# Kernel tuning notes

Hardware: AMD Instinct MI355X
Metric: run time of the kernel (lower is better)

## Reference

```python
import jax, jax.numpy as jnp
import numpy as np

N_HEADS = 16


def setup_inputs() -> dict:
    key = jax.random.key(0)
    ks = jax.random.split(key, 5)
    B, S, D = 4, 1024, 1024
    H = N_HEADS
    hs = D // H
    sc = 0.02
    return {
        "x": jax.random.normal(ks[0], (B, S, D), jnp.float32),
        "Wqkv": jax.random.normal(ks[1], (3 * D, D), jnp.float32) * sc,
        "Wout": jax.random.normal(ks[2], (D, D), jnp.float32) * sc,
        "Wpos": jax.random.normal(ks[3], (D, D), jnp.float32) * sc,
        "posn_vect_u": jnp.zeros((1, H, 1, hs), jnp.float32),
        "posn_vect_v": jnp.zeros((1, H, 1, hs), jnp.float32),
        "rel_embed": jax.random.normal(ks[4], (S, D), jnp.float32) * sc,
    }


def reference(x, Wqkv, Wout, Wpos, posn_vect_u, posn_vect_v, rel_embed):
    B, S, D = x.shape
    H = N_HEADS
    hs = D // H

    # qkv projection (torch Linear: y = x @ W.T), split into q,k,v
    qkv = x @ Wqkv.T  # [B,S,3D]
    q, k, v = jnp.split(qkv, 3, axis=-1)
    # [B,S,D] -> [B,H,S,hs]
    q = q.reshape(B, S, H, hs).transpose(0, 2, 1, 3)
    k = k.reshape(B, S, H, hs).transpose(0, 2, 1, 3)
    v = v.reshape(B, S, H, hs).transpose(0, 2, 1, 3)

    # content term: (q + u) @ k^T -> [B,H,S,S]
    attn_dots = jnp.einsum("bhqd,bhkd->bhqk", q + posn_vect_u, k)

    # relative position term (Transformer-XL style)
    rel = rel_embed[-S:] @ Wpos.T          # [S,D]
    rel = rel.T.reshape(H, hs, S)          # [H,hs,S]
    query_posn = jnp.einsum("bhqd,hdk->bhqk", q + posn_vect_v, rel)  # [B,H,S,S]

    # rel-shift gather: shifted[i,j] = query_posn[i, j - i + S - 1]
    i = jnp.arange(S)[:, None]
    j = jnp.arange(S)[None, :]
    idx = jnp.clip(j - i + S - 1, 0, S - 1)  # [S,S]; entries with j>i masked later
    shifted = jnp.take_along_axis(query_posn, idx[None, None], axis=-1)
    attn_dots = attn_dots + shifted

    # causal mask then scaled softmax (matches masked_fill then softmax(x/sqrt(hs)))
    causal = j > i  # [S,S] True above diagonal
    attn_dots = jnp.where(causal[None, None], -jnp.inf, attn_dots)
    scores = jax.nn.softmax(attn_dots / np.sqrt(hs).astype(np.float32), axis=-1)

    attn = jnp.einsum("bhqk,bhkd->bhqd", scores, v)  # [B,H,S,hs]
    out = attn.transpose(0, 2, 1, 3).reshape(B, S, D) @ Wout.T
    return out
```

## Files before the change

kernel.cpp:

```cpp
#include <hip/hip_runtime.h>

#define S_LEN 1024

typedef unsigned short u16;
using bf16x8 = __attribute__((ext_vector_type(8))) short;
using f32x4  = __attribute__((ext_vector_type(4))) float;
using u16x8  = __attribute__((ext_vector_type(8))) unsigned short;
using u16x4  = __attribute__((ext_vector_type(4))) unsigned short;
using u32x4  = __attribute__((ext_vector_type(4))) unsigned int;

__device__ __forceinline__ float bf2f(u16 b) {
  unsigned int u = ((unsigned int)b) << 16;
  return __builtin_bit_cast(float, u);
}
__device__ __forceinline__ u16 f2bf(float f) {
  unsigned int u = __builtin_bit_cast(unsigned int, f);
  unsigned int r = u + 0x7fffu + ((u >> 16) & 1u);
  return (u16)(r >> 16);
}
__device__ __forceinline__ unsigned int cvtpk(float lo, float hi) {
  unsigned int r;
  asm("v_cvt_pk_bf16_f32 %0, %1, %2" : "=v"(r) : "v"(lo), "v"(hi));
  return r;
}
__device__ __forceinline__ float fmax3(float a, float b, float c) {
  return fmaxf(fmaxf(a, b), c);
}

using gas_p = const __attribute__((address_space(1))) void*;
using las_p = __attribute__((address_space(3))) void*;
__device__ __forceinline__ void gload16(const void* g, void* l) {
  __builtin_amdgcn_global_load_lds((gas_p)g, (las_p)l, 16, 0, 0);
}

__global__ __launch_bounds__(256) void cvt_all(const float* __restrict__ x,
    const float* __restrict__ wqkv, const float* __restrict__ wout,
    const float* __restrict__ wpos, const float* __restrict__ rel,
    u16* __restrict__ xb, u16* __restrict__ wqkvb, u16* __restrict__ woutb,
    u16* __restrict__ wposb, u16* __restrict__ relb) {
  int blk = blockIdx.x;
  const float* src; u16* dst; int base;
  if (blk < 4096)      { src = x;    dst = xb;    base = blk; }
  else if (blk < 7168) { src = wqkv; dst = wqkvb; base = blk - 4096; }
  else if (blk < 8192) { src = wout; dst = woutb; base = blk - 7168; }
  else if (blk < 9216) { src = wpos; dst = wposb; base = blk - 8192; }
  else                 { src = rel;  dst = relb;  base = blk - 9216; }
  int i = (base * 256 + threadIdx.x) * 4;
  float4 v = *(const float4*)(src + i);
  u16x4 o;
  o.x = f2bf(v.x); o.y = f2bf(v.y); o.z = f2bf(v.z); o.w = f2bf(v.w);
  *(u16x4*)(dst + i) = o;
}

__global__ __launch_bounds__(256) void gemm_qkv_rel(
    const u16* __restrict__ xb, const u16* __restrict__ wqkvb,
    u16* __restrict__ qkvb, u16* __restrict__ qc, u16* __restrict__ qp,
    const float* __restrict__ uvec, const float* __restrict__ vvec,
    const u16* __restrict__ relb, const u16* __restrict__ wposb,
    u16* __restrict__ relproj) {
  __shared__ __align__(16) u16 As[2][128 * 32];
  __shared__ __align__(16) u16 Ws[2][128 * 32];
  const int t = threadIdx.x;
  const int w = t >> 6, l = t & 63;
  const int lr = l & 15, lg = l >> 4;
  const int flat = blockIdx.x;

  if (flat < 768) {
    const int xcd = flat & 7, idx = flat >> 3;
    const int bm = (xcd & 3) * 8 + (idx & 7);
    const int bn = (xcd >> 2) * 12 + (idx >> 3);
    const int wr = (w >> 1) * 64, wc = (w & 1) * 64;
    f32x4 acc[4][4];
#pragma unroll
    for (int mi = 0; mi < 4; ++mi)
#pragma unroll
      for (int ni = 0; ni < 4; ++ni) acc[mi][ni] = (f32x4){0.f, 0.f, 0.f, 0.f};
    const u16* Ab = xb + (size_t)bm * 128 * 1024;
    const u16* Wb = wqkvb + (size_t)bn * 128 * 1024;
    auto stage = [&](int k0, int buf) {
#pragma unroll
      for (int i = 0; i < 2; ++i) {
        int c = i * 256 + t;
        gload16(Ab + (size_t)(c >> 2) * 1024 + k0 + (c & 3) * 8, &As[buf][c * 8]);
      }
#pragma unroll
      for (int i = 0; i < 2; ++i) {
        int c = i * 256 + t;
        gload16(Wb + (size_t)(c >> 2) * 1024 + k0 + (c & 3) * 8, &Ws[buf][c * 8]);
      }
    };
    stage(0, 0);
    __syncthreads();
    for (int k0 = 0; k0 < 1024; k0 += 32) {
      const int cur = (k0 >> 5) & 1;
      if (k0 + 32 < 1024) stage(k0 + 32, cur ^ 1);
      bf16x8 af[4], wf[4];
#pragma unroll
      for (int mi = 0; mi < 4; ++mi)
        af[mi] = *(const bf16x8*)&As[cur][(wr + mi * 16 + lr) * 32 + lg * 8];
#pragma unroll
      for (int ni = 0; ni < 4; ++ni)
        wf[ni] = *(const bf16x8*)&Ws[cur][(wc + ni * 16 + lr) * 32 + lg * 8];
      __builtin_amdgcn_s_setprio(1);
#pragma unroll
      for (int mi = 0; mi < 4; ++mi)
#pragma unroll
        for (int ni = 0; ni < 4; ++ni)
          acc[mi][ni] = __builtin_amdgcn_mfma_f32_16x16x32_bf16(af[mi], wf[ni], acc[mi][ni], 0, 0, 0);
      __builtin_amdgcn_s_setprio(0);
      __syncthreads();
    }
#pragma unroll
    for (int mi = 0; mi < 4; ++mi)
#pragma unroll
      for (int ni = 0; ni < 4; ++ni) {
        int col = bn * 128 + wc + ni * 16 + lr;
        if (col < 1024) {
          float uu = uvec[col], vv = vvec[col];
#pragma unroll
          for (int g = 0; g < 4; ++g) {
            int row = bm * 128 + wr + mi * 16 + lg * 4 + g;
            qc[(size_t)row * 1024 + col] = f2bf((acc[mi][ni][g] + uu) * 0.125f);
            qp[(size_t)row * 1024 + col] = f2bf((acc[mi][ni][g] + vv) * 0.125f);
          }
        } else if (col < 2048) {
#pragma unroll
          for (int g = 0; g < 4; ++g) {
            int row = bm * 128 + wr + mi * 16 + lg * 4 + g;
            qkvb[(size_t)row * 3072 + col] = f2bf(acc[mi][ni][g]);
          }
        } else {
          int row0 = bm * 128 + wr + mi * 16 + lg * 4;
          int vrow = (row0 >> 10) * 1024 + (col - 2048);
          u16x4 tmp;
#pragma unroll
          for (int g = 0; g < 4; ++g) tmp[g] = f2bf(acc[mi][ni][g]);
          *(u16x4*)&qkvb[(size_t)vrow * 3072 + (row0 & 1023)] = tmp;
        }
      }
  } else {
    const int r = flat - 768;
    const int bm = r & 15, bn = r >> 4;
    const int wr = (w >> 1) * 32, wc = (w & 1) * 64;
    f32x4 acc[2][4];
#pragma unroll
    for (int mi = 0; mi < 2; ++mi)
#pragma unroll
      for (int ni = 0; ni < 4; ++ni) acc[mi][ni] = (f32x4){0.f, 0.f, 0.f, 0.f};
    const u16* Ab = relb + (size_t)bm * 64 * 1024;
    const u16* Wb = wposb + (size_t)bn * 128 * 1024;
    auto stage = [&](int k0, int buf) {
      {
        int c = t;
        gload16(Ab + (size_t)(c >> 2) * 1024 + k0 + (c & 3) * 8, &As[buf][c * 8]);
      }
#pragma unroll
      for (int i = 0; i < 2; ++i) {
        int c = i * 256 + t;
        gload16(Wb + (size_t)(c >> 2) * 1024 + k0 + (c & 3) * 8, &Ws[buf][c * 8]);
      }
    };
    stage(0, 0);
    __syncthreads();
    for (int k0 = 0; k0 < 1024; k0 += 32) {
      const int cur = (k0 >> 5) & 1;
      if (k0 + 32 < 1024) stage(k0 + 32, cur ^ 1);
      bf16x8 af[2], wf[4];
#pragma unroll
      for (int mi = 0; mi < 2; ++mi)
        af[mi] = *(const bf16x8*)&As[cur][(wr + mi * 16 + lr) * 32 + lg * 8];
#pragma unroll
      for (int ni = 0; ni < 4; ++ni)
        wf[ni] = *(const bf16x8*)&Ws[cur][(wc + ni * 16 + lr) * 32 + lg * 8];
      __builtin_amdgcn_s_setprio(1);
#pragma unroll
      for (int mi = 0; mi < 2; ++mi)
#pragma unroll
        for (int ni = 0; ni < 4; ++ni)
          acc[mi][ni] = __builtin_amdgcn_mfma_f32_16x16x32_bf16(af[mi], wf[ni], acc[mi][ni], 0, 0, 0);
      __builtin_amdgcn_s_setprio(0);
      __syncthreads();
    }
#pragma unroll
    for (int mi = 0; mi < 2; ++mi)
#pragma unroll
      for (int ni = 0; ni < 4; ++ni) {
        int col = bn * 128 + wc + ni * 16 + lr;
#pragma unroll
        for (int g = 0; g < 4; ++g) {
          int row = bm * 64 + wr + mi * 16 + lg * 4 + g;
          relproj[(size_t)row * 1024 + col] = f2bf(acc[mi][ni][g]);
        }
      }
  }
}

__global__ __launch_bounds__(256) void gemm_out(const u16* __restrict__ A,
    const u16* __restrict__ W, float* __restrict__ Yf) {
  __shared__ __align__(16) u16 As[2][64 * 32];
  __shared__ __align__(16) u16 Ws[2][128 * 32];
  const int t = threadIdx.x;
  const int w = t >> 6, l = t & 63;
  const int lr = l & 15, lg = l >> 4;
  const int flat = (int)blockIdx.y * 64 + (int)blockIdx.x;
  const int bn = flat & 7, bm = flat >> 3;
  const int wr = (w >> 1) * 32, wc = (w & 1) * 64;
  f32x4 acc[2][4];
#pragma unroll
  for (int mi = 0; mi < 2; ++mi)
#pragma unroll
    for (int ni = 0; ni < 4; ++ni) acc[mi][ni] = (f32x4){0.f, 0.f, 0.f, 0.f};
  const u16* Ab = A + (size_t)bm * 64 * 1024;
  const u16* Wb = W + (size_t)bn * 128 * 1024;
  auto stage = [&](int k0, int buf) {
    {
      int c = t;
      gload16(Ab + (size_t)(c >> 2) * 1024 + k0 + (c & 3) * 8, &As[buf][c * 8]);
    }
#pragma unroll
    for (int i = 0; i < 2; ++i) {
      int c = i * 256 + t;
      gload16(Wb + (size_t)(c >> 2) * 1024 + k0 + (c & 3) * 8, &Ws[buf][c * 8]);
    }
  };
  stage(0, 0);
  __syncthreads();
  for (int k0 = 0; k0 < 1024; k0 += 32) {
    const int cur = (k0 >> 5) & 1;
    if (k0 + 32 < 1024) stage(k0 + 32, cur ^ 1);
    bf16x8 af[2], wf[4];
#pragma unroll
    for (int mi = 0; mi < 2; ++mi)
      af[mi] = *(const bf16x8*)&As[cur][(wr + mi * 16 + lr) * 32 + lg * 8];
#pragma unroll
    for (int ni = 0; ni < 4; ++ni)
      wf[ni] = *(const bf16x8*)&Ws[cur][(wc + ni * 16 + lr) * 32 + lg * 8];
    __builtin_amdgcn_s_setprio(1);
#pragma unroll
    for (int mi = 0; mi < 2; ++mi)
#pragma unroll
      for (int ni = 0; ni < 4; ++ni)
        acc[mi][ni] = __builtin_amdgcn_mfma_f32_16x16x32_bf16(af[mi], wf[ni], acc[mi][ni], 0, 0, 0);
    __builtin_amdgcn_s_setprio(0);
    __syncthreads();
  }
#pragma unroll
  for (int mi = 0; mi < 2; ++mi)
#pragma unroll
    for (int ni = 0; ni < 4; ++ni) {
      int col = bn * 128 + wc + ni * 16 + lr;
#pragma unroll
      for (int g = 0; g < 4; ++g) {
        int row = bm * 64 + wr + mi * 16 + lg * 4 + g;
        Yf[(size_t)row * 1024 + col] = acc[mi][ni][g];
      }
    }
}

__global__ __launch_bounds__(256) void attn_fwd(
    const u16* __restrict__ qcb, const u16* __restrict__ qpb,
    const u16* __restrict__ qkv, const u16* __restrict__ relp,
    u16* __restrict__ out) {
  __shared__ __align__(16) u16 Ksb[2][4096];
  __shared__ __align__(16) u16 Vtb[2][4096];
  __shared__ __align__(16) u16 Rs3[3][4096];
  __shared__ __align__(16) float Psf[4][16][68];

  const int flat = (int)blockIdx.y * 8 + (int)blockIdx.x;
  const int wg = (flat & 7) * 64 + (flat >> 3);
  const int sub = wg & 7;
  const int bh = wg >> 3;
  const int b = bh >> 4, h = bh & 15;
  const int t = threadIdx.x;
  const int w = t >> 6, l = t & 63;
  const int lr = l & 15, lg = l >> 4;

  const u16* Kg = qkv + (size_t)b * S_LEN * 3072 + 1024 + h * 64;
  const u16* Vg = qkv + (size_t)bh * 64 * 3072;
  const u16* Rg = relp + h * 64;

  int gl4[4], cg[4];
#pragma unroll
  for (int g = 0; g < 4; ++g) {
    int ql = lg * 4 + g;
    gl4[g] = (l & 48) | ((lr - ql - 1) & 15);
    cg[g] = (lr > ql) ? 1 : 0;
  }

  for (int half = 0; half < 2; ++half) {
    const int qt = half ? sub : (15 - sub);
    const int i0 = qt * 64;
    const int nt = qt + 1;

    bf16x8 qcf[2], qpf[2];
    {
      size_t qoff = (size_t)(b * S_LEN + i0 + w * 16 + lr) * 1024 + h * 64;
      qcf[0] = *(const bf16x8*)(qcb + qoff + lg * 8);
      qcf[1] = *(const bf16x8*)(qcb + qoff + 32 + lg * 8);
      qpf[0] = *(const bf16x8*)(qpb + qoff + lg * 8);
      qpf[1] = *(const bf16x8*)(qpb + qoff + 32 + lg * 8);
    }

    auto stage_k = [&](int j0s, int buf) {
#pragma unroll
      for (int i = 0; i < 2; ++i) {
        int bK = i * 4 + w;
        int ttk = bK >> 1, kc = bK & 1;
        gload16(Kg + (size_t)(j0s + ttk * 16 + lr) * 3072 + kc * 32 + lg * 8,
                &Ksb[buf][bK * 512 + l * 8]);
      }
    };
    auto stage_v = [&](int j0s, int buf) {
#pragma unroll
      for (int i = 0; i < 2; ++i) {
        int bV = i * 4 + w;
        int dt = bV >> 1, kc = bV & 1;
        gload16(Vg + (size_t)(dt * 16 + lr) * 3072 + j0s + kc * 32 + lg * 8,
                &Vtb[buf][bV * 512 + l * 8]);
      }
    };
    auto stage_rchunk = [&](int Gloc, int slot) {
      int Gg = 15 - qt + Gloc;
#pragma unroll
      for (int i = 0; i < 2; ++i) {
        int bR = i * 4 + w;
        int btc = bR >> 1, kc = bR & 1;
        int r = Gg * 64 + btc * 16 + lr;
        r = r > S_LEN - 1 ? S_LEN - 1 : r;
        gload16(Rg + (size_t)r * 1024 + kc * 32 + lg * 8,
                &Rs3[slot][bR * 512 + l * 8]);
      }
    };

    float m_run = 0.f, l_run = 0.f;
    f32x4 o_acc[4];
#pragma unroll
    for (int dt = 0; dt < 4; ++dt) o_acc[dt] = (f32x4){0.f, 0.f, 0.f, 0.f};

    stage_k(0, 0);
    stage_v(0, 0);
    stage_rchunk(0, 0);
    stage_rchunk(1, 1);
    __syncthreads();

    int sA = 0, sB = 1, sC = 2;
    for (int kt = 0; kt < nt; ++kt) {
      const int cur = kt & 1, nxt = cur ^ 1;
      const int j0 = kt * 64;
      const int have_nxt = (kt + 1 < nt);
      if (have_nxt) {
        stage_k(j0 + 64, nxt);
        stage_v(j0 + 64, nxt);
        stage_rchunk(kt + 2, sC);
      }

      f32x4 sc[4];
      __builtin_amdgcn_s_setprio(1);
#pragma unroll
      for (int tt = 0; tt < 4; ++tt) {
        sc[tt] = (f32x4){0.f, 0.f, 0.f, 0.f};
#pragma unroll
        for (int kc = 0; kc < 2; ++kc) {
          bf16x8 kf = *(const bf16x8*)&Ksb[cur][(tt * 2 + kc) * 512 + l * 8];
          sc[tt] = __builtin_amdgcn_mfma_f32_16x16x32_bf16(qcf[kc], kf, sc[tt], 0, 0, 0);
        }
      }
      f32x4 sp[5];
#pragma unroll
      for (int u5 = 0; u5 < 5; ++u5) {
        int bt = 3 - w + u5;
        const u16* rb = (bt & 4) ? &Rs3[sB][0] : &Rs3[sA][0];
        int btc = bt & 3;
        sp[u5] = (f32x4){0.f, 0.f, 0.f, 0.f};
#pragma unroll
        for (int kc = 0; kc < 2; ++kc) {
          bf16x8 rf = *(const bf16x8*)&rb[(btc * 2 + kc) * 512 + l * 8];
          sp[u5] = __builtin_amdgcn_mfma_f32_16x16x32_bf16(qpf[kc], rf, sp[u5], 0, 0, 0);
        }
      }
      __builtin_amdgcn_s_setprio(0);

#pragma unroll
      for (int g = 0; g < 4; ++g) {
        float bp[5];
#pragma unroll
        for (int u5 = 0; u5 < 5; ++u5) bp[u5] = __shfl(sp[u5][g], gl4[g]);
#pragma unroll
        for (int tt = 0; tt < 4; ++tt)
          sc[tt][g] += cg[g] ? bp[tt + 1] : bp[tt];
      }
#pragma unroll
      for (int g = 0; g < 4; ++g)
#pragma unroll
        for (int tt = 0; tt < 4; ++tt)
          Psf[w][lg * 4 + g][tt * 16 + lr] = sc[tt][g];

      float zz[2][8];
#pragma unroll
      for (int kc = 0; kc < 2; ++kc)
#pragma unroll
        for (int h4 = 0; h4 < 2; ++h4) {
          float4 rv = *(const float4*)&Psf[w][lr][kc * 32 + lg * 8 + h4 * 4];
          zz[kc][h4 * 4 + 0] = rv.x; zz[kc][h4 * 4 + 1] = rv.y;
          zz[kc][h4 * 4 + 2] = rv.z; zz[kc][h4 * 4 + 3] = rv.w;
        }
      if (kt == nt - 1) {
        int iglob = i0 + w * 16 + lr;
#pragma unroll
        for (int kc = 0; kc < 2; ++kc)
#pragma unroll
          for (int j = 0; j < 8; ++j)
            if (j0 + kc * 32 + lg * 8 + j > iglob) zz[kc][j] = -1e30f;
      }

#pragma unroll
      for (int kc = 0; kc < 2; ++kc)
#pragma unroll
        for (int j = 0; j < 8; ++j) zz[kc][j] = __expf(zz[kc][j] - m_run);
      bf16x8 pf[2];
#pragma unroll
      for (int kc = 0; kc < 2; ++kc) {
        u32x4 pw;
#pragma unroll
        for (int j2 = 0; j2 < 4; ++j2)
          pw[j2] = cvtpk(zz[kc][j2 * 2], zz[kc][j2 * 2 + 1]);
        pf[kc] = __builtin_bit_cast(bf16x8, pw);
      }
      __builtin_amdgcn_s_setprio(1);
#pragma unroll
      for (int dt = 0; dt < 4; ++dt) {
#pragma unroll
        for (int kc = 0; kc < 2; ++kc) {
          bf16x8 vf = *(const bf16x8*)&Vtb[cur][(dt * 2 + kc) * 512 + l * 8];
          o_acc[dt] = __builtin_amdgcn_mfma_f32_16x16x32_bf16(pf[kc], vf, o_acc[dt], 0, 0, 0);
        }
      }
      __builtin_amdgcn_s_setprio(0);

      float s, em;
      {
        float a0 = zz[0][0] + zz[0][1], a1 = zz[0][2] + zz[0][3];
        float a2 = zz[0][4] + zz[0][5], a3 = zz[0][6] + zz[0][7];
        float a4 = zz[1][0] + zz[1][1], a5 = zz[1][2] + zz[1][3];
        float a6 = zz[1][4] + zz[1][5], a7 = zz[1][6] + zz[1][7];
        s = ((a0 + a1) + (a2 + a3)) + ((a4 + a5) + (a6 + a7));
        float m0 = fmax3(zz[0][0], zz[0][1], zz[0][2]);
        float m1 = fmax3(zz[0][3], zz[0][4], zz[0][5]);
        float m2 = fmax3(zz[0][6], zz[0][7], zz[1][0]);
        float m3 = fmax3(zz[1][1], zz[1][2], zz[1][3]);
        float m4 = fmax3(zz[1][4], zz[1][5], zz[1][6]);
        em = fmax3(m0, m1, zz[1][7]);
        em = fmax3(em, m2, m3);
        em = fmaxf(em, m4);
      }
      s += __shfl_xor(s, 16);
      s += __shfl_xor(s, 32);
      em = fmaxf(em, __shfl_xor(em, 16));
      em = fmaxf(em, __shfl_xor(em, 32));

      if (__all(em <= 2980.958f)) {
        l_run += s;
      } else {
        float lem = __logf(fmaxf(em, 1.f));
        float corr = __expf(-lem);
        m_run += lem;
        l_run = (l_run + s) * corr;
        float co[4];
#pragma unroll
        for (int g = 0; g < 4; ++g) co[g] = __shfl(corr, lg * 4 + g);
#pragma unroll
        for (int dt = 0; dt < 4; ++dt)
#pragma unroll
          for (int g = 0; g < 4; ++g) o_acc[dt][g] *= co[g];
      }

      __syncthreads();
      int stmp = sA; sA = sB; sB = sC; sC = stmp;
    }

    float ll[4];
#pragma unroll
    for (int g = 0; g < 4; ++g) ll[g] = __shfl(l_run, lg * 4 + g);
#pragma unroll
    for (int dt = 0; dt < 4; ++dt) {
      int col = h * 64 + dt * 16 + lr;
#pragma unroll
      for (int g = 0; g < 4; ++g) {
        int row = b * S_LEN + i0 + w * 16 + lg * 4 + g;
        out[(size_t)row * 1024 + col] = f2bf(o_acc[dt][g] / ll[g]);
      }
    }
  }
}

extern "C" void kernel_launch(void* const* d_in, const int* in_sizes, int n_in,
                              void* d_out, int out_size, void* d_ws, size_t ws_size,
                              hipStream_t stream) {
  const float* x    = (const float*)d_in[0];
  const float* Wqkv = (const float*)d_in[1];
  const float* Wout = (const float*)d_in[2];
  const float* Wpos = (const float*)d_in[3];
  const float* u    = (const float*)d_in[4];
  const float* v    = (const float*)d_in[5];
  const float* rel  = (const float*)d_in[6];
  float* out = (float*)d_out;

  u16* ws      = (u16*)d_ws;
  u16* xb      = ws;
  u16* wqkvb   = xb + 4194304;
  u16* woutb   = wqkvb + 3145728;
  u16* wposb   = woutb + 1048576;
  u16* relb    = wposb + 1048576;
  u16* qkvb    = relb + 1048576;
  u16* qcb     = qkvb + 12582912;
  u16* qpb     = qcb + 4194304;
  u16* relproj = qpb + 4194304;
  u16* attno   = relproj + 1048576;

  cvt_all<<<10240, 256, 0, stream>>>(x, Wqkv, Wout, Wpos, rel, xb, wqkvb, woutb, wposb, relb);

  gemm_qkv_rel<<<896, 256, 0, stream>>>(xb, wqkvb, qkvb, qcb, qpb, u, v, relb, wposb, relproj);
  attn_fwd<<<dim3(8, 64), 256, 0, stream>>>(qcb, qpb, qkvb, relproj, attno);
  gemm_out<<<dim3(64, 8), 256, 0, stream>>>(attno, woutb, out);
}
```

Baseline: 126.6 us.

## Software-pipeline score MFMAs one tile ahead of softmax and PV

```diff
diff --git a/kernel.cpp b/kernel.cpp
--- a/kernel.cpp
+++ b/kernel.cpp
@@ -332,68 +332,75 @@
       }
     };
 
+    f32x4 sc[4], sp[5];
+    auto compute_tile = [&](int ti) {
+      __builtin_amdgcn_s_setprio(1);
+#pragma unroll
+      for (int tt = 0; tt < 4; ++tt) {
+        sc[tt] = (f32x4){0.f, 0.f, 0.f, 0.f};
+#pragma unroll
+        for (int kc = 0; kc < 2; ++kc) {
+          bf16x8 kf = *(const bf16x8*)&Ksb[ti & 1][(tt * 2 + kc) * 512 + l * 8];
+          sc[tt] = __builtin_amdgcn_mfma_f32_16x16x32_bf16(qcf[kc], kf, sc[tt], 0, 0, 0);
+        }
+      }
+      const u16* rbA = &Rs3[ti % 3][0];
+      const u16* rbB = &Rs3[(ti + 1) % 3][0];
+#pragma unroll
+      for (int u5 = 0; u5 < 5; ++u5) {
+        int bt = 3 - w + u5;
+        const u16* rb = (bt & 4) ? rbB : rbA;
+        int btc = bt & 3;
+        sp[u5] = (f32x4){0.f, 0.f, 0.f, 0.f};
+#pragma unroll
+        for (int kc = 0; kc < 2; ++kc) {
+          bf16x8 rf = *(const bf16x8*)&rb[(btc * 2 + kc) * 512 + l * 8];
+          sp[u5] = __builtin_amdgcn_mfma_f32_16x16x32_bf16(qpf[kc], rf, sp[u5], 0, 0, 0);
+        }
+      }
+      __builtin_amdgcn_s_setprio(0);
+    };
+    auto gather_write = [&](int ti) {
+      const int j0t = ti * 64;
+      const int diag = (ti == nt - 1);
+#pragma unroll
+      for (int g = 0; g < 4; ++g) {
+        float bp[5];
+#pragma unroll
+        for (int u5 = 0; u5 < 5; ++u5) bp[u5] = __shfl(sp[u5][g], gl4[g]);
+        int ql = lg * 4 + g;
+#pragma unroll
+        for (int tt = 0; tt < 4; ++tt) {
+          float z = sc[tt][g] + (cg[g] ? bp[tt + 1] : bp[tt]);
+          if (diag && (j0t + tt * 16 + lr > i0 + w * 16 + ql)) z = -1e30f;
+          Psf[w][ql][tt * 16 + lr] = z;
+        }
+      }
+    };
+
     float m_run = 0.f, l_run = 0.f;
     f32x4 o_acc[4];
 #pragma unroll
     for (int dt = 0; dt < 4; ++dt) o_acc[dt] = (f32x4){0.f, 0.f, 0.f, 0.f};
 
     stage_k(0, 0);
+    stage_k(64, 1);
     stage_v(0, 0);
     stage_rchunk(0, 0);
     stage_rchunk(1, 1);
+    stage_rchunk(2, 2);
     __syncthreads();
-
-    int sA = 0, sB = 1, sC = 2;
+    compute_tile(0);
+    gather_write(0);
+    __syncthreads();
+
     for (int kt = 0; kt < nt; ++kt) {
-      const int cur = kt & 1, nxt = cur ^ 1;
       const int j0 = kt * 64;
-      const int have_nxt = (kt + 1 < nt);
-      if (have_nxt) {
-        stage_k(j0 + 64, nxt);
-        stage_v(j0 + 64, nxt);
-        stage_rchunk(kt + 2, sC);
-      }
-
-      f32x4 sc[4];
-      __builtin_amdgcn_s_setprio(1);
-#pragma unroll
-      for (int tt = 0; tt < 4; ++tt) {
-        sc[tt] = (f32x4){0.f, 0.f, 0.f, 0.f};
-#pragma unroll
-        for (int kc = 0; kc < 2; ++kc) {
-          bf16x8 kf = *(const bf16x8*)&Ksb[cur][(tt * 2 + kc) * 512 + l * 8];
-          sc[tt] = __builtin_amdgcn_mfma_f32_16x16x32_bf16(qcf[kc], kf, sc[tt], 0, 0, 0);
-        }
-      }
-      f32x4 sp[5];
-#pragma unroll
-      for (int u5 = 0; u5 < 5; ++u5) {
-        int bt = 3 - w + u5;
-        const u16* rb = (bt & 4) ? &Rs3[sB][0] : &Rs3[sA][0];
-        int btc = bt & 3;
-        sp[u5] = (f32x4){0.f, 0.f, 0.f, 0.f};
-#pragma unroll
-        for (int kc = 0; kc < 2; ++kc) {
-          bf16x8 rf = *(const bf16x8*)&rb[(btc * 2 + kc) * 512 + l * 8];
-          sp[u5] = __builtin_amdgcn_mfma_f32_16x16x32_bf16(qpf[kc], rf, sp[u5], 0, 0, 0);
-        }
-      }
-      __builtin_amdgcn_s_setprio(0);
-
-#pragma unroll
-      for (int g = 0; g < 4; ++g) {
-        float bp[5];
-#pragma unroll
-        for (int u5 = 0; u5 < 5; ++u5) bp[u5] = __shfl(sp[u5][g], gl4[g]);
-#pragma unroll
-        for (int tt = 0; tt < 4; ++tt)
-          sc[tt][g] += cg[g] ? bp[tt + 1] : bp[tt];
-      }
-#pragma unroll
-      for (int g = 0; g < 4; ++g)
-#pragma unroll
-        for (int tt = 0; tt < 4; ++tt)
-          Psf[w][lg * 4 + g][tt * 16 + lr] = sc[tt][g];
+      if (kt + 2 < nt) {
+        stage_k(j0 + 128, kt & 1);
+        stage_rchunk(kt + 3, kt % 3);
+      }
+      if (kt + 1 < nt) stage_v(j0 + 64, (kt + 1) & 1);
 
       float zz[2][8];
 #pragma unroll
@@ -404,15 +411,6 @@
           zz[kc][h4 * 4 + 0] = rv.x; zz[kc][h4 * 4 + 1] = rv.y;
           zz[kc][h4 * 4 + 2] = rv.z; zz[kc][h4 * 4 + 3] = rv.w;
         }
-      if (kt == nt - 1) {
-        int iglob = i0 + w * 16 + lr;
-#pragma unroll
-        for (int kc = 0; kc < 2; ++kc)
-#pragma unroll
-          for (int j = 0; j < 8; ++j)
-            if (j0 + kc * 32 + lg * 8 + j > iglob) zz[kc][j] = -1e30f;
-      }
-
 #pragma unroll
       for (int kc = 0; kc < 2; ++kc)
 #pragma unroll
@@ -426,16 +424,21 @@
           pw[j2] = cvtpk(zz[kc][j2 * 2], zz[kc][j2 * 2 + 1]);
         pf[kc] = __builtin_bit_cast(bf16x8, pw);
       }
+
+      if (kt + 1 < nt) compute_tile(kt + 1);
+
       __builtin_amdgcn_s_setprio(1);
 #pragma unroll
       for (int dt = 0; dt < 4; ++dt) {
 #pragma unroll
         for (int kc = 0; kc < 2; ++kc) {
-          bf16x8 vf = *(const bf16x8*)&Vtb[cur][(dt * 2 + kc) * 512 + l * 8];
+          bf16x8 vf = *(const bf16x8*)&Vtb[kt & 1][(dt * 2 + kc) * 512 + l * 8];
           o_acc[dt] = __builtin_amdgcn_mfma_f32_16x16x32_bf16(pf[kc], vf, o_acc[dt], 0, 0, 0);
         }
       }
       __builtin_amdgcn_s_setprio(0);
+
+      if (kt + 1 < nt) gather_write(kt + 1);
 
       float s, em;
       {
@@ -475,7 +478,6 @@
       }
 
       __syncthreads();
-      int stmp = sA; sA = sB; sB = sC; sC = stmp;
     }
 
     float ll[4];
```

Result: slower. 165.6 us (+30.8%).
